# Kernel optimization log

Measured on AMD Instinct MI355X. Metric: run time of the kernel, lower is better.

The kernel has to match this reference:

```python
import jax, jax.numpy as jnp
import numpy as np
from jax import lax

EPS = 1e-5

def _conv(x, w, b, pad):
    # NCHW conv, stride 1, symmetric padding `pad`
    y = lax.conv_general_dilated(x, w, window_strides=(1, 1),
                                 padding=[(pad, pad), (pad, pad)],
                                 dimension_numbers=('NCHW', 'OIHW', 'NCHW'))
    return y + b[None, :, None, None]

def _bn(x, gamma, beta):
    # BatchNorm2d, training mode: batch statistics over (N,H,W)
    mean = jnp.mean(x, axis=(0, 2, 3), keepdims=True)
    var = jnp.var(x, axis=(0, 2, 3), keepdims=True)
    return gamma[None, :, None, None] * (x - mean) * lax.rsqrt(var + EPS) + beta[None, :, None, None]

def setup_inputs() -> dict:
    key = jax.random.key(0)
    ks = jax.random.split(key, 8)
    B, C, H, W = 4, 256, 64, 64
    OC = 256
    s3 = 1.0 / np.sqrt(C * 9)
    s1 = 1.0 / np.sqrt(C)
    return {
        'x': jax.random.normal(ks[0], (B, C, H, W), jnp.float32),
        'Wq': jax.random.normal(ks[1], (OC, C, 3, 3), jnp.float32) * s3,
        'bq': jnp.zeros((OC,), jnp.float32),
        'gq': jnp.ones((OC,), jnp.float32),
        'betaq': jnp.zeros((OC,), jnp.float32),
        'Wk': jax.random.normal(ks[2], (OC, C, 1, 1), jnp.float32) * s1,
        'bk': jnp.zeros((OC,), jnp.float32),
        'gk': jnp.ones((OC,), jnp.float32),
        'betak': jnp.zeros((OC,), jnp.float32),
        'Wv': jax.random.normal(ks[3], (OC, C, 1, 1), jnp.float32) * s1,
        'bv': jnp.zeros((OC,), jnp.float32),
        'gv': jnp.ones((OC,), jnp.float32),
        'betav': jnp.zeros((OC,), jnp.float32),
    }

def reference(x, Wq, bq, gq, betaq, Wk, bk, gk, betak, Wv, bv, gv, betav):
    # Q: 3x3 conv, pad 1 -> (b, oc, h, w); K,V: 1x1 conv with pad 1 -> (b, oc, h+2, w+2)
    Q = _bn(_conv(x, Wq, bq, 1), gq, betaq)
    K = _bn(_conv(x, Wk, bk, 1), gk, betak)
    V = _bn(_conv(x, Wv, bv, 1), gv, betav)
    b, oc, oh, ow = Q.shape
    q = Q.reshape(b, oc, oh * ow)          # (b, c, q_tokens)
    k = K.reshape(b, oc, -1)               # (b, c, k_tokens)
    v = V.reshape(b, oc, -1)               # (b, c, k_tokens)
    scores = jnp.einsum('bck,bcq->bkq', k, q)      # (b, k_tokens, q_tokens)
    attn = jax.nn.softmax(scores, axis=1)          # softmax over key tokens (dim=1)
    out = jnp.einsum('bck,bkq->bcq', v, attn)      # (b, c, q_tokens)
    return out.reshape(b, oc, oh, ow)
```

## Files before the change

### kernel.cpp

```cpp
#include <hip/hip_runtime.h>


typedef unsigned short u16;
typedef _Float16 f16x8 __attribute__((ext_vector_type(8)));
typedef __attribute__((ext_vector_type(4))) float f32x4;
typedef __attribute__((ext_vector_type(8))) unsigned short u16x8;

__device__ __forceinline__ u16 f2h(float f) {
  _Float16 h = (_Float16)f;
  return *(const u16*)&h;
}
__device__ __forceinline__ float bf2f(u16 h) {
  return __uint_as_float(((unsigned)h) << 16);
}
__device__ __forceinline__ float ldin(const void* p, size_t i, int f32) {
  return f32 ? ((const float*)p)[i] : bf2f(((const u16*)p)[i]);
}
__device__ __forceinline__ u16 f2bf(float f) {
  unsigned u = __float_as_uint(f);
  u += 0x7fffu + ((u >> 16) & 1u);
  return (u16)(u >> 16);
}
__device__ __forceinline__ void gld16(const void* g, void* l) {
  __builtin_amdgcn_global_load_lds(
      (const __attribute__((address_space(1))) unsigned int*)g,
      (__attribute__((address_space(3))) unsigned int*)l, 16, 0, 0);
}

__global__ __launch_bounds__(256) void k_detect(const unsigned* __restrict__ w,
                                                int* __restrict__ flag) {
  __shared__ int red[4];
  int tid = threadIdx.x, cnt = 0;
#pragma unroll
  for (int j = 0; j < 8; j++) {
    unsigned e = (w[tid + j * 8192] >> 7) & 0xFFu;
    cnt += (e >= 118u && e <= 127u) ? 1 : 0;
  }
#pragma unroll
  for (int off = 32; off; off >>= 1) cnt += __shfl_down(cnt, off);
  if ((tid & 63) == 0) red[tid >> 6] = cnt;
  __syncthreads();
  if (tid == 0)
    flag[0] = (red[0] + red[1] + red[2] + red[3] < 625) ? 1 : 0;
}

__global__ __launch_bounds__(256) void k_prep(
    const void* __restrict__ x, const void* __restrict__ Wq,
    const void* __restrict__ Wk, const void* __restrict__ Wv,
    const int* __restrict__ flag, u16* __restrict__ xbTp,
    u16* __restrict__ WqB, u16* __restrict__ WkvB, float* __restrict__ bufQ) {
  __shared__ float tile[32][33];
  const int blk = blockIdx.x, tid = threadIdx.x;
  const int f32 = flag[0];
  if (blk < 4384) {
    int u = blk;
    int p0 = (u % 137) * 32;
    u /= 137;
    int c0 = (u % 8) * 32;
    int b = u / 8;
    int tx = tid & 31, ty = tid >> 5;
#pragma unroll
    for (int i = 0; i < 4; i++) {
      int c = c0 + ty + i * 8, pp = p0 + tx;
      float v = 0.f;
      if (pp < 4356) {
        int yy = pp / 66, xx = pp - yy * 66;
        if (yy >= 1 && yy <= 64 && xx >= 1 && xx <= 64)
          v = ldin(x, ((size_t)b * 256 + c) * 4096 + (yy - 1) * 64 + (xx - 1), f32);
      }
      tile[ty + i * 8][tx] = v;
    }
    __syncthreads();
#pragma unroll
    for (int i = 0; i < 4; i++) {
      int pp = p0 + ty + i * 8;
      if (pp >= 4356) continue;
      xbTp[((size_t)b * 4356 + pp) * 256 + c0 + tx] = f2h(tile[tx][ty + i * 8]);
    }
  } else if (blk < 6688) {
    int idx = (blk - 4384) * 256 + tid;
    int oc = idx / 2304, rem = idx - oc * 2304;
    int tap = rem >> 8, c = rem & 255;
    WqB[idx] = f2h(ldin(Wq, oc * 2304 + c * 9 + tap, f32));
    f32x4* bz = (f32x4*)bufQ;
    for (int i = idx; i < 1048576; i += 589824)
      bz[i] = (f32x4){0.f, 0.f, 0.f, 0.f};
  } else {
    int idx = (blk - 6688) * 256 + tid;
    int m = idx >> 8, c = idx & 255;
    float w = (m < 256) ? ldin(Wk, m * 256 + c, f32)
                        : ldin(Wv, (m - 256) * 256 + c, f32);
    WkvB[idx] = f2h(w);
  }
}

template <int EPI>
__device__ __forceinline__ void gemm_body(
    const u16* __restrict__ A, const u16* __restrict__ Bt,
    float* __restrict__ C, u16* lA, u16* lB, int N, int K, int tapBase,
    int kChunk, int sw1, int sw2, int lin, int kz) {
  int xcd = lin & 7, per = lin >> 3;
  int tm = per % sw1;
  int tn = xcd * sw2 + per / sw1;
  int k0 = 0, k1 = K;
  if (kChunk) {
    k0 = kz * kChunk;
    k1 = min(k0 + kChunk, K);
  }
  const int tid = threadIdx.x, wave = tid >> 6, lane = tid & 63;
  const int sr = lane >> 3;
  const int scw = (lane & 7) ^ sr;
  const int wm = (wave >> 1) * 64, wn = (wave & 1) * 64;
  const int r16 = lane & 15, q = lane >> 4;
  const u16* gA = A + (size_t)(tm * 128 + wave * 32 + sr) * K + scw * 8;
  int pyI[4], pxI[4];
  size_t bOffI[4];
#pragma unroll
  for (int i = 0; i < 4; i++) {
    int n = tn * 128 + wave * 32 + i * 8 + sr;
    int bb = n >> 12, pix = n & 4095;
    pyI[i] = pix >> 6;
    pxI[i] = pix & 63;
    bOffI[i] = (size_t)bb * 4356;
  }
  f32x4 acc[4][4] = {};

  for (int kt = k0; kt < k1; kt += 64) {
    int tap = tapBase + (kt >> 8);
    int chunk = kt & 255;
    int dy = tap / 3, dx = tap - dy * 3;
#pragma unroll
    for (int i = 0; i < 4; i++) {
      gld16(gA + (size_t)(i * 8) * K + kt, &lA[(wave * 32 + i * 8) * 64]);
      int spix = (pyI[i] + dy) * 66 + pxI[i] + dx;
      gld16(Bt + (bOffI[i] + spix) * 256 + chunk + scw * 8,
            &lB[(wave * 32 + i * 8) * 64]);
    }
    __syncthreads();
#pragma unroll
    for (int ks = 0; ks < 64; ks += 32) {
      f16x8 af[4], bfr[4];
#pragma unroll
      for (int f = 0; f < 4; f++) {
        int ma = wm + f * 16 + r16;
        int g = (ks >> 3) + q;
        af[f] = *(const f16x8*)&lA[ma * 64 + ((g ^ (ma & 7)) << 3)];
        int nb = wn + f * 16 + r16;
        bfr[f] = *(const f16x8*)&lB[nb * 64 + ((g ^ (nb & 7)) << 3)];
      }
#pragma unroll
      for (int fi = 0; fi < 4; fi++)
#pragma unroll
        for (int fj = 0; fj < 4; fj++)
          acc[fi][fj] = __builtin_amdgcn_mfma_f32_16x16x32_f16(
              af[fi], bfr[fj], acc[fi][fj], 0, 0, 0);
    }
    __syncthreads();
  }

  const int colB = tn * 128 + wn + r16;
  const int rowB = tm * 128 + wm + q * 4;
  if (EPI == 0) {
#pragma unroll
    for (int fi = 0; fi < 4; fi++)
#pragma unroll
      for (int r = 0; r < 4; r++) {
        size_t ro = (size_t)(rowB + fi * 16 + r) * N;
#pragma unroll
        for (int fj = 0; fj < 4; fj++) C[ro + colB + fj * 16] = acc[fi][fj][r];
      }
  } else {
#pragma unroll
    for (int fi = 0; fi < 4; fi++)
#pragma unroll
      for (int r = 0; r < 4; r++) {
        size_t ro = (size_t)(rowB + fi * 16 + r) * N;
#pragma unroll
        for (int fj = 0; fj < 4; fj++)
          atomicAdd(&C[ro + colB + fj * 16], acc[fi][fj][r]);
      }
  }
}

__global__ __launch_bounds__(256, 3) void k_convs(
    const u16* __restrict__ WqB, const u16* __restrict__ WkvB,
    const u16* __restrict__ xbTp, float* __restrict__ bufQ,
    float* __restrict__ bufKV) {
  __shared__ u16 lA[128 * 64];
  __shared__ u16 lB[128 * 64];
  int idx = blockIdx.x;
  if (idx < 768)
    gemm_body<1>(WqB, xbTp, bufQ, lA, lB, 16384, 2304, 0, 768, 2, 16,
                 idx & 255, idx >> 8);
  else
    gemm_body<0>(WkvB, xbTp, bufKV, lA, lB, 16384, 256, 4, 0, 4, 16,
                 idx - 768, 0);
}

__global__ __launch_bounds__(256) void k_stats(
    const float* __restrict__ bufQ, const float* __restrict__ bufKV,
    const void* __restrict__ gq, const void* __restrict__ betaq,
    const void* __restrict__ gk, const void* __restrict__ betak,
    const void* __restrict__ gv, const void* __restrict__ betav,
    const int* __restrict__ flag, float* __restrict__ nrm) {
  int f32 = flag[0];
  int ch = blockIdx.x, t = blockIdx.y, tid = threadIdx.x;
  const float* row = (t == 0) ? bufQ + (size_t)ch * 16384
                              : bufKV + (size_t)(t == 1 ? ch : 256 + ch) * 16384;
  const f32x4* row4 = (const f32x4*)row;
  float s = 0.f, ss = 0.f;
  for (int i = tid; i < 4096; i += 256) {
    f32x4 v = row4[i];
    s += v[0] + v[1] + v[2] + v[3];
    ss += v[0] * v[0] + v[1] * v[1] + v[2] * v[2] + v[3] * v[3];
  }
#pragma unroll
  for (int off = 32; off; off >>= 1) {
    s += __shfl_down(s, off);
    ss += __shfl_down(ss, off);
  }
  __shared__ float ls[4], lss[4];
  if ((tid & 63) == 0) {
    ls[tid >> 6] = s;
    lss[tid >> 6] = ss;
  }
  __syncthreads();
  if (tid == 0) {
    s = ls[0] + ls[1] + ls[2] + ls[3];
    ss = lss[0] + lss[1] + lss[2] + lss[3];
    float cnt = (t == 0) ? 16384.f : 17424.f;
    float mean = s / cnt;
    float var = fmaxf(ss / cnt - mean * mean, 0.f);
    const void* g = (t == 0) ? gq : (t == 1 ? gk : gv);
    const void* be = (t == 0) ? betaq : (t == 1 ? betak : betav);
    float sc = ldin(g, ch, f32) * rsqrtf(var + 1e-5f);
    nrm[(t * 256 + ch) * 2] = sc;
    nrm[(t * 256 + ch) * 2 + 1] = ldin(be, ch, f32) - mean * sc;
  }
}

__global__ __launch_bounds__(256) void k_norm(
    const float* __restrict__ bufQ, const float* __restrict__ bufKV,
    const float* __restrict__ nrm, u16* __restrict__ qTs,
    u16* __restrict__ kTs, u16* __restrict__ vP) {
  __shared__ u16 th[32][33];
  const int blk = blockIdx.x, tid = threadIdx.x;
  const int tx = tid & 31, ty = tid >> 5;
  if (blk < 4096) {
    int u = blk;
    int q0 = (u % 128) * 32;
    u /= 128;
    int c0 = (u % 8) * 32;
    int b = u / 8;
#pragma unroll
    for (int i = 0; i < 4; i++) {
      int c = c0 + ty + i * 8;
      float sc = nrm[c * 2], sh = nrm[c * 2 + 1];
      th[ty + i * 8][tx] =
          f2h(bufQ[(size_t)c * 16384 + b * 4096 + q0 + tx] * sc + sh);
    }
    __syncthreads();
#pragma unroll
    for (int i = 0; i < 4; i++)
      qTs[((size_t)b * 4096 + q0 + ty + i * 8) * 256 + c0 + tx] =
          th[tx][ty + i * 8];
  } else if (blk < 8576) {
    int u = blk - 4096;
    int k0 = (u % 140) * 32;
    u /= 140;
    int c0 = (u % 8) * 32;
    int b = u / 8;
#pragma unroll
    for (int i = 0; i < 4; i++) {
      int c = c0 + ty + i * 8;
      int kt = k0 + tx;
      float v = 0.f;
      if (kt < 4356) {
        float sc = nrm[(256 + c) * 2], sh = nrm[(256 + c) * 2 + 1];
        int yy = kt / 66, xx = kt - yy * 66;
        if (yy >= 1 && yy <= 64 && xx >= 1 && xx <= 64)
          v = bufKV[(size_t)c * 16384 + b * 4096 + (yy - 1) * 64 + (xx - 1)] * sc + sh;
        else
          v = sh;
      }
      th[ty + i * 8][tx] = f2h(v);
    }
    __syncthreads();
#pragma unroll
    for (int i = 0; i < 4; i++)
      kTs[((size_t)b * 4480 + k0 + ty + i * 8) * 256 + c0 + tx] =
          th[tx][ty + i * 8];
  } else {
    int idx = (blk - 8576) * 256 + tid;
    int kt8 = idx % 560;
    int rem = idx / 560;
    int ch = rem & 255, b = rem >> 8;
    int kt0 = kt8 * 8;
    float sc = nrm[(512 + ch) * 2], sh = nrm[(512 + ch) * 2 + 1];
    u16x8 v8;
#pragma unroll
    for (int j = 0; j < 8; j++) {
      int kt = kt0 + j;
      float v = 0.f;
      if (kt < 4356) {
        int yy = kt / 66, xx = kt - yy * 66;
        if (yy >= 1 && yy <= 64 && xx >= 1 && xx <= 64)
          v = bufKV[(size_t)(256 + ch) * 16384 + b * 4096 + (yy - 1) * 64 + (xx - 1)] * sc + sh;
        else
          v = sh;
      }
      v8[j] = f2h(v);
    }
    *(u16x8*)&vP[((size_t)b * 256 + ch) * 4480 + kt0] = v8;
  }
}

__global__ __launch_bounds__(256, 2) void k_flash(
    const u16* __restrict__ qTs, const u16* __restrict__ kTs,
    const u16* __restrict__ vP, float* __restrict__ Op,
    float* __restrict__ ml) {
  __shared__ u16 lS[2][16384];
  __shared__ u16 lP[64 * 64];
  __shared__ float lFac[64];
  const int lin = blockIdx.x;
  const int xcd = lin & 7, per = lin >> 3;
  const int h = xcd & 1, b = xcd >> 1;
  const int qt0 = per * 64;
  const int tid = threadIdx.x, wave = tid >> 6, lane = tid & 63;
  const int sr = lane >> 3, scw = (lane & 7) ^ sr;
  const int r16 = lane & 15, q = lane >> 4;

  const u16* gQ = qTs + ((size_t)b * 4096 + qt0 + wave * 16 + r16) * 256;
  f16x8 aq[8];
#pragma unroll
  for (int kk = 0; kk < 8; kk++) aq[kk] = *(const f16x8*)&gQ[kk * 32 + q * 8];
  asm volatile("s_waitcnt vmcnt(0)" ::: "memory");

  const u16* gK = kTs + (size_t)b * 4480 * 256 + (size_t)(wave * 32 + sr) * 256 + scw * 8;
  const u16* gV = vP + ((size_t)b * 256 + wave * 64 + sr) * 4480 + scw * 8;

#define STAGE_K(buf, kt, c2)                                                 \
  {                                                                          \
    _Pragma("unroll") for (int i = 0; i < 4; i++) {                          \
      const u16* src = gK + (size_t)((kt) + i * 8) * 256 + (c2) * 128;       \
      gld16(src, &lS[buf][(wave * 32 + i * 8) * 64]);                        \
      gld16(src + 64, &lS[buf][8192 + (wave * 32 + i * 8) * 64]);            \
    }                                                                        \
  }
#define STAGE_V(buf, kt, vc)                                                 \
  {                                                                          \
    _Pragma("unroll") for (int i = 0; i < 8; i++)                            \
        gld16(gV + (size_t)(i * 8) * 4480 + (kt) + (vc) * 64,                \
              &lS[buf][(wave * 64 + i * 8) * 64]);                           \
  }
#define WAITB(n)                                                             \
  asm volatile("s_waitcnt vmcnt(" #n ") lgkmcnt(0)" ::: "memory");           \
  __builtin_amdgcn_s_barrier();                                              \
  __builtin_amdgcn_sched_barrier(0);
#define CLOSEB()                                                             \
  __builtin_amdgcn_sched_barrier(0);                                         \
  asm volatile("s_waitcnt lgkmcnt(0)" ::: "memory");                         \
  __builtin_amdgcn_s_barrier();

  f32x4 acc_o[4][4];
#pragma unroll
  for (int mt = 0; mt < 4; mt++)
#pragma unroll
    for (int fj = 0; fj < 4; fj++) acc_o[mt][fj] = (f32x4){0.f, 0.f, 0.f, 0.f};
  f32x4 m_v = {-3e38f, -3e38f, -3e38f, -3e38f};
  f32x4 l_v = {0.f, 0.f, 0.f, 0.f};

  const int ktBeg = h ? 2304 : 0, ktEnd = h ? 4480 : 2304;
  STAGE_K(0, ktBeg, 0);
  for (int kt0 = ktBeg; kt0 < ktEnd; kt0 += 128) {
    f32x4 acc_s[8];
#pragma unroll
    for (int i = 0; i < 8; i++) acc_s[i] = (f32x4){0.f, 0.f, 0.f, 0.f};
    STAGE_K(1, kt0, 1);
    WAITB(8);
    __builtin_amdgcn_s_setprio(1);
#pragma unroll
    for (int kcL = 0; kcL < 2; kcL++)
#pragma unroll
      for (int ks = 0; ks < 64; ks += 32)
#pragma unroll
        for (int fj = 0; fj < 8; fj++) {
          int nb = fj * 16 + r16;
          int g = (ks >> 3) + q;
          f16x8 bf = *(const f16x8*)&lS[0][kcL * 8192 + nb * 64 + ((g ^ (nb & 7)) << 3)];
          acc_s[fj] = __builtin_amdgcn_mfma_f32_16x16x32_f16(
              aq[kcL * 2 + (ks >> 5)], bf, acc_s[fj], 0, 0, 0);
        }
    __builtin_amdgcn_s_setprio(0);
    CLOSEB();
    STAGE_V(0, kt0, 0);
    WAITB(8);
    __builtin_amdgcn_s_setprio(1);
#pragma unroll
    for (int kcL = 0; kcL < 2; kcL++)
#pragma unroll
      for (int ks = 0; ks < 64; ks += 32)
#pragma unroll
        for (int fj = 0; fj < 8; fj++) {
          int nb = fj * 16 + r16;
          int g = (ks >> 3) + q;
          f16x8 bf = *(const f16x8*)&lS[1][kcL * 8192 + nb * 64 + ((g ^ (nb & 7)) << 3)];
          acc_s[fj] = __builtin_amdgcn_mfma_f32_16x16x32_f16(
              aq[4 + kcL * 2 + (ks >> 5)], bf, acc_s[fj], 0, 0, 0);
        }
    __builtin_amdgcn_s_setprio(0);
    CLOSEB();
    STAGE_V(1, kt0, 1);
    if (kt0 + 128 > 4356) {
#pragma unroll
      for (int fj = 0; fj < 8; fj++)
        if (kt0 + fj * 16 + r16 >= 4356)
          acc_s[fj] = (f32x4){-1e30f, -1e30f, -1e30f, -1e30f};
    }
    f32x4 pm = acc_s[0];
#pragma unroll
    for (int fj = 1; fj < 8; fj++)
#pragma unroll
      for (int rr = 0; rr < 4; rr++) pm[rr] = fmaxf(pm[rr], acc_s[fj][rr]);
#pragma unroll
    for (int d = 1; d < 16; d <<= 1)
#pragma unroll
      for (int rr = 0; rr < 4; rr++)
        pm[rr] = fmaxf(pm[rr], __shfl_xor(pm[rr], d));
    int need = !__all(pm[0] - m_v[0] <= 8.f && pm[1] - m_v[1] <= 8.f &&
                      pm[2] - m_v[2] <= 8.f && pm[3] - m_v[3] <= 8.f);
    f32x4 fac = {1.f, 1.f, 1.f, 1.f};
    if (need) {
#pragma unroll
      for (int rr = 0; rr < 4; rr++) {
        float mn = fmaxf(m_v[rr], pm[rr]);
        fac[rr] = __expf(m_v[rr] - mn);
        m_v[rr] = mn;
        l_v[rr] *= fac[rr];
      }
    }
    if (r16 == 0) *(f32x4*)&lFac[wave * 16 + q * 4] = fac;
    _Float16 hq[4][4];
    f32x4 rs = {0.f, 0.f, 0.f, 0.f};
#pragma unroll
    for (int fj = 0; fj < 8; fj++)
#pragma unroll
      for (int rr = 0; rr < 4; rr++) {
        _Float16 hp = (_Float16)__expf(acc_s[fj][rr] - m_v[rr]);
        rs[rr] += (float)hp;
        int row = wave * 16 + q * 4 + rr;
        if (fj < 4) {
          int c8 = fj * 2 + (r16 >> 3);
          lP[row * 64 + (((c8 ^ (row & 7)) << 3) | (r16 & 7))] = *(const u16*)&hp;
        } else {
          hq[fj - 4][rr] = hp;
        }
      }
#pragma unroll
    for (int d = 1; d < 16; d <<= 1)
#pragma unroll
      for (int rr = 0; rr < 4; rr++) rs[rr] += __shfl_xor(rs[rr], d);
#pragma unroll
    for (int rr = 0; rr < 4; rr++) l_v[rr] += rs[rr];
    WAITB(8);
    f32x4 facv[4];
#pragma unroll
    for (int mt = 0; mt < 4; mt++)
      facv[mt] = *(const f32x4*)&lFac[mt * 16 + q * 4];
#pragma unroll
    for (int mt = 0; mt < 4; mt++)
#pragma unroll
      for (int fj = 0; fj < 4; fj++)
#pragma unroll
        for (int rr = 0; rr < 4; rr++) acc_o[mt][fj][rr] *= facv[mt][rr];
    __builtin_amdgcn_s_setprio(1);
#pragma unroll
    for (int ks = 0; ks < 64; ks += 32) {
      int k8 = (ks >> 3) + q;
      f16x8 ap[4];
#pragma unroll
      for (int mt = 0; mt < 4; mt++)
        ap[mt] = *(const f16x8*)&lP[(mt * 16 + r16) * 64 + ((k8 ^ (r16 & 7)) << 3)];
#pragma unroll
      for (int fj = 0; fj < 4; fj++) {
        int cr = wave * 64 + fj * 16 + r16;
        f16x8 bv = *(const f16x8*)&lS[0][cr * 64 + ((k8 ^ (cr & 7)) << 3)];
#pragma unroll
        for (int mt = 0; mt < 4; mt++)
          acc_o[mt][fj] = __builtin_amdgcn_mfma_f32_16x16x32_f16(
              ap[mt], bv, acc_o[mt][fj], 0, 0, 0);
      }
    }
    __builtin_amdgcn_s_setprio(0);
    CLOSEB();
#pragma unroll
    for (int fj = 0; fj < 4; fj++)
#pragma unroll
      for (int rr = 0; rr < 4; rr++) {
        int row = wave * 16 + q * 4 + rr;
        int c8 = fj * 2 + (r16 >> 3);
        lP[row * 64 + (((c8 ^ (row & 7)) << 3) | (r16 & 7))] =
            *(const u16*)&hq[fj][rr];
      }
    if (kt0 + 128 < ktEnd) {
      STAGE_K(0, kt0 + 128, 0);
      WAITB(8);
    } else {
      WAITB(0);
    }
    __builtin_amdgcn_s_setprio(1);
#pragma unroll
    for (int ks = 0; ks < 64; ks += 32) {
      int k8 = (ks >> 3) + q;
      f16x8 ap[4];
#pragma unroll
      for (int mt = 0; mt < 4; mt++)
        ap[mt] = *(const f16x8*)&lP[(mt * 16 + r16) * 64 + ((k8 ^ (r16 & 7)) << 3)];
#pragma unroll
      for (int fj = 0; fj < 4; fj++) {
        int cr = wave * 64 + fj * 16 + r16;
        f16x8 bv = *(const f16x8*)&lS[1][cr * 64 + ((k8 ^ (cr & 7)) << 3)];
#pragma unroll
        for (int mt = 0; mt < 4; mt++)
          acc_o[mt][fj] = __builtin_amdgcn_mfma_f32_16x16x32_f16(
              ap[mt], bv, acc_o[mt][fj], 0, 0, 0);
      }
    }
    __builtin_amdgcn_s_setprio(0);
    CLOSEB();
  }
#undef STAGE_K
#undef STAGE_V
#undef WAITB
#undef CLOSEB
  size_t obase = ((size_t)(h * 4 + b) * 4096 + qt0) * 256;
#pragma unroll
  for (int mt = 0; mt < 4; mt++)
#pragma unroll
    for (int rr = 0; rr < 4; rr++) {
      size_t rowo = obase + (size_t)(mt * 16 + q * 4 + rr) * 256;
#pragma unroll
      for (int fj = 0; fj < 4; fj++)
        Op[rowo + wave * 64 + fj * 16 + r16] = acc_o[mt][fj][rr];
    }
  if (r16 == 0) {
    int base = (h * 4 + b) * 4096 + qt0 + wave * 16 + q * 4;
    *(f32x4*)&ml[base] = m_v;
    *(f32x4*)&ml[32768 + base] = l_v;
  }
}

__global__ __launch_bounds__(256) void k_merge(const float* __restrict__ Op,
                                               const float* __restrict__ ml,
                                               const int* __restrict__ flag,
                                               void* __restrict__ out) {
  __shared__ float th[32][33];
  int b = blockIdx.z, qt0 = blockIdx.x * 32, c0 = blockIdx.y * 32;
  int tx = threadIdx.x, ty = threadIdx.y;
#pragma unroll
  for (int i = 0; i < 4; i++) {
    int qt = qt0 + ty + i * 8;
    float m0 = ml[b * 4096 + qt], m1 = ml[(4 + b) * 4096 + qt];
    float l0 = ml[32768 + b * 4096 + qt], l1 = ml[32768 + (4 + b) * 4096 + qt];
    float M = fmaxf(m0, m1);
    float e0 = __expf(m0 - M), e1 = __expf(m1 - M);
    float inv = 1.f / (l0 * e0 + l1 * e1);
    float v = (Op[((size_t)b * 4096 + qt) * 256 + c0 + tx] * e0 +
               Op[((size_t)(4 + b) * 4096 + qt) * 256 + c0 + tx] * e1) * inv;
    v = (v == v) ? v : 0.f;
    th[ty + i * 8][tx] = v;
  }
  __syncthreads();
#pragma unroll
  for (int i = 0; i < 4; i++) {
    int c = c0 + ty + i * 8, qt = qt0 + tx;
    float v = th[tx][ty + i * 8];
    size_t oidx = ((size_t)b * 256 + c) * 4096 + qt;
    if (flag[0])
      ((float*)out)[oidx] = v;
    else
      ((u16*)out)[oidx] = f2bf(v);
  }
}

extern "C" void kernel_launch(void* const* d_in, const int* in_sizes, int n_in,
                              void* d_out, int out_size, void* d_ws, size_t ws_size,
                              hipStream_t stream) {
  const void* x = d_in[0];
  const void* Wq = d_in[1];
  const void* gq = d_in[3];
  const void* betaq = d_in[4];
  const void* Wk = d_in[5];
  const void* gk = d_in[7];
  const void* betak = d_in[8];
  const void* Wv = d_in[9];
  const void* gv = d_in[11];
  const void* betav = d_in[12];

  char* ws = (char*)d_ws;
  int* flag = (int*)ws;
  u16* xbTp = (u16*)(ws + 256);
  u16* WqB = (u16*)(ws + 8921344);
  u16* WkvB = (u16*)(ws + 10100992);
  float* bufQ = (float*)(ws + 10363136);
  float* bufKV = (float*)(ws + 27140352);
  u16* qTs = (u16*)(ws + 60694784);
  u16* kTs = (u16*)(ws + 69083392);
  u16* vP = (u16*)(ws + 78258432);
  float* nrm = (float*)(ws + 87433472);
  float* Opart = (float*)(ws + 256);
  float* mlbuf = (float*)(ws + 33554688);

  k_detect<<<1, 256, 0, stream>>>((const unsigned*)Wq, flag);
  k_prep<<<7200, 256, 0, stream>>>(x, Wq, Wk, Wv, flag, xbTp, WqB, WkvB, bufQ);
  k_convs<<<1280, 256, 0, stream>>>(WqB, WkvB, xbTp, bufQ, bufKV);
  k_stats<<<dim3(256, 3), 256, 0, stream>>>(bufQ, bufKV, gq, betaq, gk, betak,
                                            gv, betav, flag, nrm);
  k_norm<<<10816, 256, 0, stream>>>(bufQ, bufKV, nrm, qTs, kTs, vP);
  k_flash<<<512, 256, 0, stream>>>(qTs, kTs, vP, Opart, mlbuf);
  k_merge<<<dim3(128, 8, 4), dim3(32, 8), 0, stream>>>(Opart, mlbuf, flag,
                                                       d_out);
}
```

Measured before the change: 321.5 us.

## Double-buffer conv GEMM LDS tiles with K-step 32 and async prefetch

Restructures the conv implicit-GEMM main loop into a two-stage software pipeline. K-tiles shrink from 64 to 32, LDS is split into two buffers of the same total size, and the next tile is prefetched via global_load_lds while the current one is computed, using manual vmcnt waits and raw s_barrier calls. The swizzle and staging layout are rewritten to match the 32-wide rows. This aims to hide global load latency behind MFMA work, at the cost of twice as many barriers per K and more loop overhead.

Result: faster. 311.1 us (median of 2 runs) (-3.3%).

```diff
diff --git a/kernel.cpp b/kernel.cpp
--- a/kernel.cpp
+++ b/kernel.cpp
@@ -108,16 +108,17 @@
     k1 = min(k0 + kChunk, K);
   }
   const int tid = threadIdx.x, wave = tid >> 6, lane = tid & 63;
-  const int sr = lane >> 3;
-  const int scw = (lane & 7) ^ sr;
+  const int sr4 = lane >> 2;
+  const int scw4 = (lane & 3) ^ (sr4 >> 2);
   const int wm = (wave >> 1) * 64, wn = (wave & 1) * 64;
   const int r16 = lane & 15, q = lane >> 4;
-  const u16* gA = A + (size_t)(tm * 128 + wave * 32 + sr) * K + scw * 8;
-  int pyI[4], pxI[4];
-  size_t bOffI[4];
-#pragma unroll
-  for (int i = 0; i < 4; i++) {
-    int n = tn * 128 + wave * 32 + i * 8 + sr;
+  const int qsw = (r16 >> 2) & 3;
+  const u16* gA = A + (size_t)(tm * 128 + wave * 32 + sr4) * K + scw4 * 8;
+  int pyI[2], pxI[2];
+  size_t bOffI[2];
+#pragma unroll
+  for (int i = 0; i < 2; i++) {
+    int n = tn * 128 + wave * 32 + i * 16 + sr4;
     int bb = n >> 12, pix = n & 4095;
     pyI[i] = pix >> 6;
     pxI[i] = pix & 63;
@@ -125,37 +126,52 @@
   }
   f32x4 acc[4][4] = {};
 
-  for (int kt = k0; kt < k1; kt += 64) {
+  auto stage = [&](int buf, int kt) {
     int tap = tapBase + (kt >> 8);
     int chunk = kt & 255;
     int dy = tap / 3, dx = tap - dy * 3;
 #pragma unroll
-    for (int i = 0; i < 4; i++) {
-      gld16(gA + (size_t)(i * 8) * K + kt, &lA[(wave * 32 + i * 8) * 64]);
+    for (int i = 0; i < 2; i++) {
+      gld16(gA + (size_t)(i * 16) * K + kt,
+            &lA[buf * 4096 + (wave * 32 + i * 16) * 32]);
       int spix = (pyI[i] + dy) * 66 + pxI[i] + dx;
-      gld16(Bt + (bOffI[i] + spix) * 256 + chunk + scw * 8,
-            &lB[(wave * 32 + i * 8) * 64]);
-    }
-    __syncthreads();
-#pragma unroll
-    for (int ks = 0; ks < 64; ks += 32) {
-      f16x8 af[4], bfr[4];
-#pragma unroll
-      for (int f = 0; f < 4; f++) {
-        int ma = wm + f * 16 + r16;
-        int g = (ks >> 3) + q;
-        af[f] = *(const f16x8*)&lA[ma * 64 + ((g ^ (ma & 7)) << 3)];
-        int nb = wn + f * 16 + r16;
-        bfr[f] = *(const f16x8*)&lB[nb * 64 + ((g ^ (nb & 7)) << 3)];
-      }
-#pragma unroll
-      for (int fi = 0; fi < 4; fi++)
-#pragma unroll
-        for (int fj = 0; fj < 4; fj++)
-          acc[fi][fj] = __builtin_amdgcn_mfma_f32_16x16x32_f16(
-              af[fi], bfr[fj], acc[fi][fj], 0, 0, 0);
-    }
-    __syncthreads();
+      gld16(Bt + (bOffI[i] + spix) * 256 + chunk + scw4 * 8,
+            &lB[buf * 4096 + (wave * 32 + i * 16) * 32]);
+    }
+  };
+  auto compute = [&](int buf) {
+    f16x8 af[4], bfr[4];
+#pragma unroll
+    for (int f = 0; f < 4; f++) {
+      int ma = wm + f * 16 + r16;
+      af[f] = *(const f16x8*)&lA[buf * 4096 + ma * 32 + ((q ^ qsw) << 3)];
+      int nb = wn + f * 16 + r16;
+      bfr[f] = *(const f16x8*)&lB[buf * 4096 + nb * 32 + ((q ^ qsw) << 3)];
+    }
+#pragma unroll
+    for (int fi = 0; fi < 4; fi++)
+#pragma unroll
+      for (int fj = 0; fj < 4; fj++)
+        acc[fi][fj] = __builtin_amdgcn_mfma_f32_16x16x32_f16(
+            af[fi], bfr[fj], acc[fi][fj], 0, 0, 0);
+  };
+
+  stage(0, k0);
+  int cur = 0;
+  for (int kt = k0; kt < k1; kt += 32) {
+    if (kt + 32 < k1) {
+      stage(cur ^ 1, kt + 32);
+      asm volatile("s_waitcnt vmcnt(4)" ::: "memory");
+    } else {
+      asm volatile("s_waitcnt vmcnt(0)" ::: "memory");
+    }
+    __builtin_amdgcn_s_barrier();
+    __builtin_amdgcn_sched_barrier(0);
+    compute(cur);
+    __builtin_amdgcn_sched_barrier(0);
+    asm volatile("s_waitcnt lgkmcnt(0)" ::: "memory");
+    __builtin_amdgcn_s_barrier();
+    cur ^= 1;
   }
 
   const int colB = tn * 128 + wn + r16;
@@ -186,8 +202,8 @@
     const u16* __restrict__ WqB, const u16* __restrict__ WkvB,
     const u16* __restrict__ xbTp, float* __restrict__ bufQ,
     float* __restrict__ bufKV) {
-  __shared__ u16 lA[128 * 64];
-  __shared__ u16 lB[128 * 64];
+  __shared__ u16 lA[2 * 128 * 32];
+  __shared__ u16 lB[2 * 128 * 32];
   int idx = blockIdx.x;
   if (idx < 768)
     gemm_body<1>(WqB, xbTp, bufQ, lA, lB, 16384, 2304, 0, 768, 2, 16,
```
